# Performance work log

Hardware: AMD Instinct MI355X
Metric: run time of the kernel (lower is better)

The kernel has to match this reference:

```python
import jax, jax.numpy as jnp
import numpy as np

TAU = 1.0
NUM_CENTROIDS = 8
COMMITMENT_COST = 0.25


def setup_inputs() -> dict:
    key = jax.random.key(0)
    kx, kc = jax.random.split(key)
    B, T, D = 8, 2048, 512
    K = 4096  # codebook_size
    x = jax.random.normal(kx, (B, T, D), dtype=jnp.float32)
    # variance_scaling(1.0, fan_in, uniform): limit = sqrt(3/D)
    limit = np.sqrt(3.0 / D).astype(np.float32)
    codebook = jax.random.uniform(kc, (K, D), dtype=jnp.float32, minval=-limit, maxval=limit)
    return {"x": x, "codebook": codebook}


def _squared_euclidean_distance(a, b):
    # a: [N, D], b: [K, D] -> [N, K]
    a2 = jnp.sum(a * a, axis=-1, keepdims=True)          # [N, 1]
    b2 = jnp.sum(b * b, axis=-1)                          # [K]
    ab = a @ b.T                                          # [N, K]
    return a2 - 2.0 * ab + b2


def reference(x, codebook):
    B, T, D = x.shape
    K = codebook.shape[0]
    flat = x.reshape(-1, D)
    distances = _squared_euclidean_distance(flat, codebook).reshape(B, T, K)
    weights = jax.nn.softmax(-distances / TAU, axis=-1)
    top_weights, top_indices = jax.lax.top_k(weights, NUM_CENTROIDS)  # [B,T,k]
    top_weights = top_weights / jnp.sum(top_weights, axis=-1, keepdims=True)
    # decode_ids: weighted sum of gathered codebook rows (== one-hot einsum)
    gathered = jnp.take(codebook, top_indices, axis=0)                # [B,T,k,D]
    quantized = jnp.einsum('btk,btkd->btd', top_weights, gathered)
    # train=True losses (entropy_loss_ratio == 0 -> skipped)
    e_latent_loss = jnp.mean((jax.lax.stop_gradient(quantized) - x) ** 2) * COMMITMENT_COST
    q_latent_loss = jnp.mean((quantized - jax.lax.stop_gradient(x)) ** 2)
    loss = e_latent_loss.astype(jnp.float32) + q_latent_loss.astype(jnp.float32)
    # straight-through estimator
    quantized = x + jax.lax.stop_gradient(quantized - x)
    return quantized, loss
```

## Files before the change

### kernel.cpp

```cpp
#include <hip/hip_runtime.h>
#include <hip/hip_bf16.h>
#include <stdint.h>

#define D_DIM 512
#define K_CB  4096
#define N_TOK 16384
#define TOPK  8

#define TOKB  64
#define NPASS 4

typedef __attribute__((ext_vector_type(8)))  short          bf16x8;
typedef __attribute__((ext_vector_type(8)))  unsigned short us8;
typedef __attribute__((ext_vector_type(16))) float          f32x16;
typedef __attribute__((ext_vector_type(4)))  float          f32x4;

__device__ __forceinline__ unsigned short f2bf(float f) {
    union { float f; unsigned u; } v; v.f = f;
    unsigned r = (v.u + 0x7fffu + ((v.u >> 16) & 1u)) >> 16;
    return (unsigned short)r;
}

__device__ __forceinline__ void inskey(unsigned int k, unsigned int (&ts)[8]) {
    #pragma unroll
    for (int q = 0; q < 8; ++q) {
        unsigned int hi = ts[q] > k ? ts[q] : k;
        unsigned int lo = ts[q] > k ? k : ts[q];
        ts[q] = hi; k = lo;
    }
}

__global__ __launch_bounds__(256) void conv_cb_kernel(
    const float* __restrict__ cb, unsigned short* __restrict__ cbf,
    float* __restrict__ cnorm, float* __restrict__ loss,
    unsigned int* __restrict__ ticket) {
    __shared__ unsigned short ls[32 * 512];
    const int t = threadIdx.x, g32 = blockIdx.x;
    if (g32 == 0 && t == 0) { *loss = 0.f; *ticket = 0u; }
    const int row32 = t >> 3;
    float sq = 0.f;
    #pragma unroll
    for (int i = 0; i < 8; ++i) {
        const int gg = (t & 7) + 8 * i;
        const float* src = cb + ((size_t)(g32 * 32 + row32)) * D_DIM + gg * 8;
        float4 a = ((const float4*)src)[0], b = ((const float4*)src)[1];
        ushort4 o0, o1;
        o0.x = f2bf(a.x); o0.y = f2bf(a.y); o0.z = f2bf(a.z); o0.w = f2bf(a.w);
        o1.x = f2bf(b.x); o1.y = f2bf(b.y); o1.z = f2bf(b.z); o1.w = f2bf(b.w);
        const int li = (gg >> 1) * 512 + ((gg & 1) * 32 + row32) * 8;
        *(ushort4*)&ls[li]     = o0;
        *(ushort4*)&ls[li + 4] = o1;
        sq += a.x*a.x + a.y*a.y + a.z*a.z + a.w*a.w
            + b.x*b.x + b.y*b.y + b.z*b.z + b.w*b.w;
    }
    sq += __shfl_down(sq, 4, 8);
    sq += __shfl_down(sq, 2, 8);
    sq += __shfl_down(sq, 1, 8);
    if ((t & 7) == 0) cnorm[g32 * 32 + row32] = sq;
    __syncthreads();
    #pragma unroll
    for (int j = 0; j < 8; ++j) {
        const int s = j * 256 + t;
        *(ushort4*)(cbf + (size_t)g32 * 16384 + s * 8)     = *(const ushort4*)&ls[s * 8];
        *(ushort4*)(cbf + (size_t)g32 * 16384 + s * 8 + 4) = *(const ushort4*)&ls[s * 8 + 4];
    }
}

__global__ __launch_bounds__(1024) void vq_fused(
    const float* __restrict__ x, const float* __restrict__ cb,
    const unsigned short* __restrict__ cbf, const float* __restrict__ cnorm,
    float* __restrict__ out, float* __restrict__ loss_acc,
    unsigned int* __restrict__ ticket)
{
    __shared__ union {
        unsigned short xs[TOKB * D_DIM];
        unsigned int keys[256 * 64];
    } u;
    __shared__ float ncn[K_CB];
    __shared__ unsigned int pk[64 * 32];
    __shared__ int   tki[TOKB * TOPK];
    __shared__ float tks[TOKB * TOPK];
    __shared__ float tkw[TOKB * TOPK];
    __shared__ float redbuf[16];

    const int t    = threadIdx.x;
    const int lane = t & 63;
    const int w    = t >> 6;
    const int m32  = lane & 31;
    const int half = lane >> 5;
    const int tok0 = blockIdx.x * TOKB;

    #pragma unroll
    for (int i = 0; i < 2; ++i) {
        const int gg0 = i * 32 + w * 2;
        const float* src = x + (size_t)(tok0 + lane) * D_DIM + gg0 * 8;
        f32x4 v0 = ((const f32x4*)src)[0], v1 = ((const f32x4*)src)[1];
        f32x4 v2 = ((const f32x4*)src)[2], v3 = ((const f32x4*)src)[3];
        us8 o0, o1;
        o0[0] = f2bf(2.f*v0.x); o0[1] = f2bf(2.f*v0.y); o0[2] = f2bf(2.f*v0.z); o0[3] = f2bf(2.f*v0.w);
        o0[4] = f2bf(2.f*v1.x); o0[5] = f2bf(2.f*v1.y); o0[6] = f2bf(2.f*v1.z); o0[7] = f2bf(2.f*v1.w);
        o1[0] = f2bf(2.f*v2.x); o1[1] = f2bf(2.f*v2.y); o1[2] = f2bf(2.f*v2.z); o1[3] = f2bf(2.f*v2.w);
        o1[4] = f2bf(2.f*v3.x); o1[5] = f2bf(2.f*v3.y); o1[6] = f2bf(2.f*v3.z); o1[7] = f2bf(2.f*v3.w);
        const int di = (lane >> 5) * 16384 + (gg0 >> 1) * 512 + (lane & 31) * 8;
        *(us8*)&u.xs[di]       = o0;
        *(us8*)&u.xs[di + 256] = o1;
    }
    {
        float4 v = ((const float4*)cnorm)[t];
        float4 nv = {64.f - v.x, 64.f - v.y, 64.f - v.z, 64.f - v.w};
        *(float4*)&ncn[t * 4] = nv;
    }
    __syncthreads();

    unsigned int ts0[8], ts1[8];
    #pragma unroll
    for (int i = 0; i < 8; ++i) { ts0[i] = 0u; ts1[i] = 0u; }

    const char* cf = (const char*)cbf;
    for (int p = 0; p < NPASS; ++p) {
        const int ga = p * 32 + w * 2;
        f32x16 a00, a01, a10, a11;
        #pragma unroll
        for (int g = 0; g < 4; ++g) {
            float4 n0 = *(const float4*)&ncn[ga * 32 + g * 8 + 4 * half];
            float4 n1 = *(const float4*)&ncn[ga * 32 + 32 + g * 8 + 4 * half];
            a00[g*4+0]=n0.x; a00[g*4+1]=n0.y; a00[g*4+2]=n0.z; a00[g*4+3]=n0.w;
            a01[g*4+0]=n0.x; a01[g*4+1]=n0.y; a01[g*4+2]=n0.z; a01[g*4+3]=n0.w;
            a10[g*4+0]=n1.x; a10[g*4+1]=n1.y; a10[g*4+2]=n1.z; a10[g*4+3]=n1.w;
            a11[g*4+0]=n1.x; a11[g*4+1]=n1.y; a11[g*4+2]=n1.z; a11[g*4+3]=n1.w;
        }
        const char* ab = cf + (size_t)ga * 32768 + (size_t)lane * 16;
        #pragma unroll 8
        for (int ks = 0; ks < 32; ++ks) {
            bf16x8 A0 = *(const bf16x8*)(ab + (size_t)ks * 1024);
            bf16x8 A1 = *(const bf16x8*)(ab + 32768 + (size_t)ks * 1024);
            bf16x8 B0 = *(const bf16x8*)&u.xs[ks * 512 + lane * 8];
            bf16x8 B1 = *(const bf16x8*)&u.xs[16384 + ks * 512 + lane * 8];
            a00 = __builtin_amdgcn_mfma_f32_32x32x16_bf16(A0, B0, a00, 0, 0, 0);
            a01 = __builtin_amdgcn_mfma_f32_32x32x16_bf16(A0, B1, a01, 0, 0, 0);
            a10 = __builtin_amdgcn_mfma_f32_32x32x16_bf16(A1, B0, a10, 0, 0, 0);
            a11 = __builtin_amdgcn_mfma_f32_32x32x16_bf16(A1, B1, a11, 0, 0, 0);
        }
        const unsigned int K0 = 4095u - (unsigned int)(ga * 32) - 4u * (unsigned int)half;
        #pragma unroll
        for (int r = 0; r < 16; ++r) {
            const unsigned int cr = (unsigned int)((r & 3) + 8 * (r >> 2));
            inskey((__float_as_uint(a00[r]) & 0xFFFFF000u) | (K0 - cr),       ts0);
            inskey((__float_as_uint(a01[r]) & 0xFFFFF000u) | (K0 - cr),       ts1);
            inskey((__float_as_uint(a10[r]) & 0xFFFFF000u) | (K0 - 32u - cr), ts0);
            inskey((__float_as_uint(a11[r]) & 0xFFFFF000u) | (K0 - 32u - cr), ts1);
        }
    }

    __syncthreads();
    {
        const int kk = (w * 2 + half) * 8;
        #pragma unroll
        for (int e = 0; e < 8; ++e) {
            u.keys[(kk + e) * 64 + m32]      = ts0[e];
            u.keys[(kk + e) * 64 + 32 + m32] = ts1[e];
        }
    }
    __syncthreads();
    if (t < 256) {
        const int token = t >> 2, sub = t & 3;
        unsigned int bs[8];
        #pragma unroll
        for (int i = 0; i < 8; ++i) bs[i] = 0u;
        #pragma unroll 4
        for (int k = 0; k < 64; ++k) inskey(u.keys[(sub * 64 + k) * 64 + token], bs);
        #pragma unroll
        for (int e = 0; e < 8; ++e) pk[token * 32 + sub * 8 + e] = bs[e];
    }
    __syncthreads();
    if (t < TOKB) {
        unsigned int bs[8];
        #pragma unroll
        for (int i = 0; i < 8; ++i) bs[i] = 0u;
        #pragma unroll 4
        for (int k = 0; k < 32; ++k) inskey(pk[t * 32 + k], bs);
        #pragma unroll
        for (int r = 0; r < TOPK; ++r) tki[t * TOPK + r] = 4095 - (int)(bs[r] & 0xFFFu);
    }
    __syncthreads();
    {
        const int token = t >> 4, e = (t >> 1) & 7, dh = t & 1;
        const int idx = tki[token * TOPK + e];
        const float4* xr = (const float4*)(x + (size_t)(tok0 + token) * D_DIM) + dh * 64;
        const float4* cr = (const float4*)(cb + (size_t)idx * D_DIM) + dh * 64;
        float dot = 0.f;
        #pragma unroll 4
        for (int i = 0; i < 64; ++i) {
            float4 xv = xr[i], cv = cr[i];
            dot += xv.x*cv.x + xv.y*cv.y + xv.z*cv.z + xv.w*cv.w;
        }
        dot += __shfl_xor(dot, 1, 64);
        if (dh == 0) tks[token * TOPK + e] = 2.f * dot - cnorm[idx];
    }
    __syncthreads();
    if (t < TOKB) {
        float m = -1e38f;
        #pragma unroll
        for (int e = 0; e < TOPK; ++e) m = fmaxf(m, tks[t*TOPK+e]);
        float sum = 0.f, wv[TOPK];
        #pragma unroll
        for (int e = 0; e < TOPK; ++e) { wv[e] = __expf(tks[t*TOPK+e] - m); sum += wv[e]; }
        const float inv = 1.f / sum;
        #pragma unroll
        for (int e = 0; e < TOPK; ++e) tkw[t*TOPK+e] = wv[e] * inv;
    }
    __syncthreads();
    float lsum = 0.f;
    #pragma unroll 1
    for (int it = 0; it < (TOKB * (D_DIM / 4)) / 1024; ++it) {
        const int p = it * 1024 + t;
        const int token = p >> 7, d4 = p & 127;
        float4 q = {0.f, 0.f, 0.f, 0.f};
        #pragma unroll
        for (int e = 0; e < TOPK; ++e) {
            const float wv = tkw[token * TOPK + e];
            const int  idx = tki[token * TOPK + e];
            const float4 cv = ((const float4*)cb)[(size_t)idx * (D_DIM / 4) + d4];
            q.x += wv * cv.x; q.y += wv * cv.y; q.z += wv * cv.z; q.w += wv * cv.w;
        }
        const size_t go = (size_t)(tok0 + token) * (D_DIM / 4) + d4;
        f32x4 xv = __builtin_nontemporal_load((const f32x4*)x + go);
        const float ex = q.x - xv.x, ey = q.y - xv.y, ez = q.z - xv.z, ew = q.w - xv.w;
        lsum += ex*ex + ey*ey + ez*ez + ew*ew;
        f32x4 qv = {q.x, q.y, q.z, q.w};
        __builtin_nontemporal_store(qv, (f32x4*)out + go);
    }
    #pragma unroll
    for (int off = 32; off > 0; off >>= 1) lsum += __shfl_down(lsum, off, 64);
    if (lane == 0) redbuf[w] = lsum;
    __syncthreads();
    if (t == 0) {
        float s = 0.f;
        #pragma unroll
        for (int i = 0; i < 16; ++i) s += redbuf[i];
        atomicAdd(loss_acc, s);
        __threadfence();
        unsigned int prev = atomicAdd(ticket, 1u);
        if (prev == (unsigned int)(gridDim.x - 1)) {
            __threadfence();
            float total = atomicAdd(loss_acc, 0.f);
            out[(size_t)N_TOK * D_DIM] = 1.25f * total / (float)((size_t)N_TOK * D_DIM);
        }
    }
}

extern "C" void kernel_launch(void* const* d_in, const int* in_sizes, int n_in,
                              void* d_out, int out_size, void* d_ws, size_t ws_size,
                              hipStream_t stream) {
    const float* x  = (const float*)d_in[0];
    const float* cb = (const float*)d_in[1];
    float* out = (float*)d_out;

    char* ws = (char*)d_ws;
    unsigned short* cbf    = (unsigned short*)ws;
    float*          cnorm  = (float*)(ws + 4194304);
    float*          loss   = (float*)(ws + 4210688);
    unsigned int*   ticket = (unsigned int*)(ws + 4210752);

    conv_cb_kernel<<<128, 256, 0, stream>>>(cb, cbf, cnorm, loss, ticket);
    vq_fused<<<N_TOK / TOKB, 1024, 0, stream>>>(x, cb, cbf, cnorm, out, loss, ticket);
}
```

Before: 255.4 us.

## Switch distance GEMM to scaled FP8 MFMA with 16-candidate fp32 rerank

Result: slower. 285.7 us (+11.9%).

```diff
diff --git a/kernel.cpp b/kernel.cpp
--- a/kernel.cpp
+++ b/kernel.cpp
@@ -1,5 +1,4 @@
 #include <hip/hip_runtime.h>
-#include <hip/hip_bf16.h>
 #include <stdint.h>
 
 #define D_DIM 512
@@ -9,21 +8,17 @@
 
 #define TOKB  64
 #define NPASS 4
-
-typedef __attribute__((ext_vector_type(8)))  short          bf16x8;
-typedef __attribute__((ext_vector_type(8)))  unsigned short us8;
-typedef __attribute__((ext_vector_type(16))) float          f32x16;
-typedef __attribute__((ext_vector_type(4)))  float          f32x4;
-
-__device__ __forceinline__ unsigned short f2bf(float f) {
-    union { float f; unsigned u; } v; v.f = f;
-    unsigned r = (v.u + 0x7fffu + ((v.u >> 16) & 1u)) >> 16;
-    return (unsigned short)r;
-}
-
-__device__ __forceinline__ void inskey(unsigned int k, unsigned int (&ts)[8]) {
+#define NSEL  16
+
+typedef __attribute__((ext_vector_type(4)))  int    i32x4;
+typedef __attribute__((ext_vector_type(8)))  int    i32x8;
+typedef __attribute__((ext_vector_type(16))) float  f32x16;
+typedef __attribute__((ext_vector_type(4)))  float  f32x4;
+
+template<int N>
+__device__ __forceinline__ void inskey(unsigned int k, unsigned int (&ts)[N]) {
     #pragma unroll
-    for (int q = 0; q < 8; ++q) {
+    for (int q = 0; q < N; ++q) {
         unsigned int hi = ts[q] > k ? ts[q] : k;
         unsigned int lo = ts[q] > k ? k : ts[q];
         ts[q] = hi; k = lo;
@@ -31,56 +26,54 @@
 }
 
 __global__ __launch_bounds__(256) void conv_cb_kernel(
-    const float* __restrict__ cb, unsigned short* __restrict__ cbf,
+    const float* __restrict__ cb, unsigned char* __restrict__ cbf8,
     float* __restrict__ cnorm, float* __restrict__ loss,
     unsigned int* __restrict__ ticket) {
-    __shared__ unsigned short ls[32 * 512];
-    const int t = threadIdx.x, g32 = blockIdx.x;
-    if (g32 == 0 && t == 0) { *loss = 0.f; *ticket = 0u; }
-    const int row32 = t >> 3;
+    const int t = threadIdx.x, g = blockIdx.x;
+    if (g == 0 && t == 0) { *loss = 0.f; *ticket = 0u; }
+    const int r = t >> 3, s = t & 7;
+    const float* src = cb + ((size_t)(g * 32 + r)) * D_DIM + s * 64;
     float sq = 0.f;
+    unsigned int d[16];
     #pragma unroll
-    for (int i = 0; i < 8; ++i) {
-        const int gg = (t & 7) + 8 * i;
-        const float* src = cb + ((size_t)(g32 * 32 + row32)) * D_DIM + gg * 8;
-        float4 a = ((const float4*)src)[0], b = ((const float4*)src)[1];
-        ushort4 o0, o1;
-        o0.x = f2bf(a.x); o0.y = f2bf(a.y); o0.z = f2bf(a.z); o0.w = f2bf(a.w);
-        o1.x = f2bf(b.x); o1.y = f2bf(b.y); o1.z = f2bf(b.z); o1.w = f2bf(b.w);
-        const int li = (gg >> 1) * 512 + ((gg & 1) * 32 + row32) * 8;
-        *(ushort4*)&ls[li]     = o0;
-        *(ushort4*)&ls[li + 4] = o1;
-        sq += a.x*a.x + a.y*a.y + a.z*a.z + a.w*a.w
-            + b.x*b.x + b.y*b.y + b.z*b.z + b.w*b.w;
+    for (int i = 0; i < 16; ++i) {
+        float4 v = ((const float4*)src)[i];
+        sq += v.x*v.x + v.y*v.y + v.z*v.z + v.w*v.w;
+        int dd = __builtin_amdgcn_cvt_pk_fp8_f32(64.f * v.x, 64.f * v.y, 0, false);
+        dd     = __builtin_amdgcn_cvt_pk_fp8_f32(64.f * v.z, 64.f * v.w, dd, true);
+        d[i] = (unsigned int)dd;
     }
     sq += __shfl_down(sq, 4, 8);
     sq += __shfl_down(sq, 2, 8);
     sq += __shfl_down(sq, 1, 8);
-    if ((t & 7) == 0) cnorm[g32 * 32 + row32] = sq;
-    __syncthreads();
-    #pragma unroll
-    for (int j = 0; j < 8; ++j) {
-        const int s = j * 256 + t;
-        *(ushort4*)(cbf + (size_t)g32 * 16384 + s * 8)     = *(const ushort4*)&ls[s * 8];
-        *(ushort4*)(cbf + (size_t)g32 * 16384 + s * 8 + 4) = *(const ushort4*)&ls[s * 8 + 4];
-    }
+    if (s == 0) cnorm[g * 32 + r] = sq;
+    unsigned char* dst = cbf8 + (size_t)g * 16384 + (size_t)s * 2048;
+    i32x4 w0 = {(int)d[0],  (int)d[1],  (int)d[2],  (int)d[3]};
+    i32x4 w1 = {(int)d[4],  (int)d[5],  (int)d[6],  (int)d[7]};
+    i32x4 w2 = {(int)d[8],  (int)d[9],  (int)d[10], (int)d[11]};
+    i32x4 w3 = {(int)d[12], (int)d[13], (int)d[14], (int)d[15]};
+    *(i32x4*)(dst +        (size_t)r * 16)        = w0;
+    *(i32x4*)(dst + 1024 + (size_t)r * 16)        = w1;
+    *(i32x4*)(dst +        (size_t)(32 + r) * 16) = w2;
+    *(i32x4*)(dst + 1024 + (size_t)(32 + r) * 16) = w3;
 }
 
 __global__ __launch_bounds__(1024) void vq_fused(
     const float* __restrict__ x, const float* __restrict__ cb,
-    const unsigned short* __restrict__ cbf, const float* __restrict__ cnorm,
+    const unsigned char* __restrict__ cbf8, const float* __restrict__ cnorm,
     float* __restrict__ out, float* __restrict__ loss_acc,
     unsigned int* __restrict__ ticket)
 {
     __shared__ union {
-        unsigned short xs[TOKB * D_DIM];
-        unsigned int keys[256 * 64];
+        unsigned char xs8[TOKB * D_DIM];
+        unsigned int  keys[256 * 64];
     } u;
     __shared__ float ncn[K_CB];
-    __shared__ unsigned int pk[64 * 32];
-    __shared__ int   tki[TOKB * TOPK];
-    __shared__ float tks[TOKB * TOPK];
+    __shared__ unsigned int pk[64 * 64];
+    __shared__ int   tki[TOKB * NSEL];
+    __shared__ float tks[TOKB * NSEL];
     __shared__ float tkw[TOKB * TOPK];
+    __shared__ int   tkif[TOKB * TOPK];
     __shared__ float redbuf[16];
 
     const int t    = threadIdx.x;
@@ -90,24 +83,29 @@
     const int half = lane >> 5;
     const int tok0 = blockIdx.x * TOKB;
 
-    #pragma unroll
-    for (int i = 0; i < 2; ++i) {
-        const int gg0 = i * 32 + w * 2;
-        const float* src = x + (size_t)(tok0 + lane) * D_DIM + gg0 * 8;
-        f32x4 v0 = ((const f32x4*)src)[0], v1 = ((const f32x4*)src)[1];
-        f32x4 v2 = ((const f32x4*)src)[2], v3 = ((const f32x4*)src)[3];
-        us8 o0, o1;
-        o0[0] = f2bf(2.f*v0.x); o0[1] = f2bf(2.f*v0.y); o0[2] = f2bf(2.f*v0.z); o0[3] = f2bf(2.f*v0.w);
-        o0[4] = f2bf(2.f*v1.x); o0[5] = f2bf(2.f*v1.y); o0[6] = f2bf(2.f*v1.z); o0[7] = f2bf(2.f*v1.w);
-        o1[0] = f2bf(2.f*v2.x); o1[1] = f2bf(2.f*v2.y); o1[2] = f2bf(2.f*v2.z); o1[3] = f2bf(2.f*v2.w);
-        o1[4] = f2bf(2.f*v3.x); o1[5] = f2bf(2.f*v3.y); o1[6] = f2bf(2.f*v3.z); o1[7] = f2bf(2.f*v3.w);
-        const int di = (lane >> 5) * 16384 + (gg0 >> 1) * 512 + (lane & 31) * 8;
-        *(us8*)&u.xs[di]       = o0;
-        *(us8*)&u.xs[di + 256] = o1;
+    {
+        const int token = t >> 4, c = t & 15;
+        const int s2 = c >> 1, lh = c & 1;
+        const f32x4* src = (const f32x4*)(x + (size_t)(tok0 + token) * D_DIM + c * 32);
+        unsigned int d[8];
+        #pragma unroll
+        for (int i = 0; i < 8; ++i) {
+            f32x4 v = src[i];
+            int dd = __builtin_amdgcn_cvt_pk_fp8_f32(16.f * v.x, 16.f * v.y, 0, false);
+            dd     = __builtin_amdgcn_cvt_pk_fp8_f32(16.f * v.z, 16.f * v.w, dd, true);
+            d[i] = (unsigned int)dd;
+        }
+        const int lf = lh * 32 + (token & 31);
+        unsigned char* base = u.xs8 + (token >> 5) * 16384 + s2 * 2048 + lf * 16;
+        i32x4 lo = {(int)d[0], (int)d[1], (int)d[2], (int)d[3]};
+        i32x4 hi = {(int)d[4], (int)d[5], (int)d[6], (int)d[7]};
+        *(i32x4*)(base)        = lo;
+        *(i32x4*)(base + 1024) = hi;
     }
     {
         float4 v = ((const float4*)cnorm)[t];
-        float4 nv = {64.f - v.x, 64.f - v.y, 64.f - v.z, 64.f - v.w};
+        float4 nv = {32768.f - 512.f * v.x, 32768.f - 512.f * v.y,
+                     32768.f - 512.f * v.z, 32768.f - 512.f * v.w};
         *(float4*)&ncn[t * 4] = nv;
     }
     __syncthreads();
@@ -116,8 +114,11 @@
     #pragma unroll
     for (int i = 0; i < 8; ++i) { ts0[i] = 0u; ts1[i] = 0u; }
 
-    const char* cf = (const char*)cbf;
-    for (int p = 0; p < NPASS; ++p) {
+    const char* ab0 = (const char*)cbf8 + (size_t)(w * 2) * 16384 + (size_t)lane * 16;
+    const unsigned char* pb = u.xs8 + lane * 16;
+
+    for (int pp = 0; pp < NPASS; ++pp) {
+        const int p  = (pp + w) & 3;
         const int ga = p * 32 + w * 2;
         f32x16 a00, a01, a10, a11;
         #pragma unroll
@@ -129,18 +130,32 @@
             a10[g*4+0]=n1.x; a10[g*4+1]=n1.y; a10[g*4+2]=n1.z; a10[g*4+3]=n1.w;
             a11[g*4+0]=n1.x; a11[g*4+1]=n1.y; a11[g*4+2]=n1.z; a11[g*4+3]=n1.w;
         }
-        const char* ab = cf + (size_t)ga * 32768 + (size_t)lane * 16;
-        #pragma unroll 8
-        for (int ks = 0; ks < 32; ++ks) {
-            bf16x8 A0 = *(const bf16x8*)(ab + (size_t)ks * 1024);
-            bf16x8 A1 = *(const bf16x8*)(ab + 32768 + (size_t)ks * 1024);
-            bf16x8 B0 = *(const bf16x8*)&u.xs[ks * 512 + lane * 8];
-            bf16x8 B1 = *(const bf16x8*)&u.xs[16384 + ks * 512 + lane * 8];
-            a00 = __builtin_amdgcn_mfma_f32_32x32x16_bf16(A0, B0, a00, 0, 0, 0);
-            a01 = __builtin_amdgcn_mfma_f32_32x32x16_bf16(A0, B1, a01, 0, 0, 0);
-            a10 = __builtin_amdgcn_mfma_f32_32x32x16_bf16(A1, B0, a10, 0, 0, 0);
-            a11 = __builtin_amdgcn_mfma_f32_32x32x16_bf16(A1, B1, a11, 0, 0, 0);
-        }
+        const char* ab = ab0 + (size_t)p * 524288;
+        __builtin_amdgcn_s_setprio(1);
+        #pragma unroll
+        for (int s = 0; s < 8; ++s) {
+            i32x4 al0 = *(const i32x4*)(ab + s * 2048);
+            i32x4 ah0 = *(const i32x4*)(ab + s * 2048 + 1024);
+            i32x4 al1 = *(const i32x4*)(ab + s * 2048 + 16384);
+            i32x4 ah1 = *(const i32x4*)(ab + s * 2048 + 17408);
+            i32x4 bl0 = *(const i32x4*)(pb + s * 2048);
+            i32x4 bh0 = *(const i32x4*)(pb + s * 2048 + 1024);
+            i32x4 bl1 = *(const i32x4*)(pb + s * 2048 + 16384);
+            i32x4 bh1 = *(const i32x4*)(pb + s * 2048 + 17408);
+            i32x8 A0 = __builtin_shufflevector(al0, ah0, 0,1,2,3,4,5,6,7);
+            i32x8 A1 = __builtin_shufflevector(al1, ah1, 0,1,2,3,4,5,6,7);
+            i32x8 B0 = __builtin_shufflevector(bl0, bh0, 0,1,2,3,4,5,6,7);
+            i32x8 B1 = __builtin_shufflevector(bl1, bh1, 0,1,2,3,4,5,6,7);
+            a00 = __builtin_amdgcn_mfma_scale_f32_32x32x64_f8f6f4(
+                      A0, B0, a00, 0, 0, 0, 0x7F7F7F7F, 0, 0x7F7F7F7F);
+            a01 = __builtin_amdgcn_mfma_scale_f32_32x32x64_f8f6f4(
+                      A0, B1, a01, 0, 0, 0, 0x7F7F7F7F, 0, 0x7F7F7F7F);
+            a10 = __builtin_amdgcn_mfma_scale_f32_32x32x64_f8f6f4(
+                      A1, B0, a10, 0, 0, 0, 0x7F7F7F7F, 0, 0x7F7F7F7F);
+            a11 = __builtin_amdgcn_mfma_scale_f32_32x32x64_f8f6f4(
+                      A1, B1, a11, 0, 0, 0, 0x7F7F7F7F, 0, 0x7F7F7F7F);
+        }
+        __builtin_amdgcn_s_setprio(0);
         const unsigned int K0 = 4095u - (unsigned int)(ga * 32) - 4u * (unsigned int)half;
         #pragma unroll
         for (int r = 0; r < 16; ++r) {
@@ -164,50 +179,87 @@
     __syncthreads();
     if (t < 256) {
         const int token = t >> 2, sub = t & 3;
-        unsigned int bs[8];
-        #pragma unroll
-        for (int i = 0; i < 8; ++i) bs[i] = 0u;
-        #pragma unroll 4
+        unsigned int bs[16];
+        #pragma unroll
+        for (int i = 0; i < 16; ++i) bs[i] = 0u;
+        #pragma unroll 2
         for (int k = 0; k < 64; ++k) inskey(u.keys[(sub * 64 + k) * 64 + token], bs);
         #pragma unroll
-        for (int e = 0; e < 8; ++e) pk[token * 32 + sub * 8 + e] = bs[e];
+        for (int e = 0; e < 16; ++e) pk[token * 64 + sub * 16 + e] = bs[e];
+    }
+    __syncthreads();
+    if (t < TOKB) {
+        unsigned int bs[NSEL];
+        #pragma unroll
+        for (int i = 0; i < NSEL; ++i) bs[i] = 0u;
+        #pragma unroll 2
+        for (int k = 0; k < 64; ++k) inskey(pk[t * 64 + k], bs);
+        #pragma unroll
+        for (int r = 0; r < NSEL; ++r) tki[t * NSEL + r] = 4095 - (int)(bs[r] & 0xFFFu);
+    }
+    __syncthreads();
+    {
+        const int token = t >> 4, sl = t & 15;
+        const f32x4* xr = (const f32x4*)(x + (size_t)(tok0 + token) * D_DIM);
+        f32x4 xv[8];
+        #pragma unroll
+        for (int i = 0; i < 8; ++i) xv[i] = xr[sl + 16 * i];
+        #pragma unroll
+        for (int hh = 0; hh < 2; ++hh) {
+            float pd[8];
+            #pragma unroll
+            for (int e = 0; e < 8; ++e) {
+                const int idx = tki[token * NSEL + hh * 8 + e];
+                const f32x4* cr = (const f32x4*)(cb + (size_t)idx * D_DIM);
+                float dot = 0.f;
+                #pragma unroll
+                for (int i = 0; i < 8; ++i) {
+                    f32x4 cv = cr[sl + 16 * i];
+                    dot += xv[i].x*cv.x + xv[i].y*cv.y + xv[i].z*cv.z + xv[i].w*cv.w;
+                }
+                pd[e] = dot;
+            }
+            #pragma unroll
+            for (int e = 0; e < 8; ++e) {
+                pd[e] += __shfl_down(pd[e], 8, 16);
+                pd[e] += __shfl_down(pd[e], 4, 16);
+                pd[e] += __shfl_down(pd[e], 2, 16);
+                pd[e] += __shfl_down(pd[e], 1, 16);
+            }
+            if (sl == 0) {
+                #pragma unroll
+                for (int e = 0; e < 8; ++e)
+                    tks[token * NSEL + hh * 8 + e] =
+                        2.f * pd[e] - cnorm[tki[token * NSEL + hh * 8 + e]];
+            }
+        }
     }
     __syncthreads();
     if (t < TOKB) {
         unsigned int bs[8];
         #pragma unroll
         for (int i = 0; i < 8; ++i) bs[i] = 0u;
-        #pragma unroll 4
-        for (int k = 0; k < 32; ++k) inskey(pk[t * 32 + k], bs);
-        #pragma unroll
-        for (int r = 0; r < TOPK; ++r) tki[t * TOPK + r] = 4095 - (int)(bs[r] & 0xFFFu);
-    }
-    __syncthreads();
-    {
-        const int token = t >> 4, e = (t >> 1) & 7, dh = t & 1;
-        const int idx = tki[token * TOPK + e];
-        const float4* xr = (const float4*)(x + (size_t)(tok0 + token) * D_DIM) + dh * 64;
-        const float4* cr = (const float4*)(cb + (size_t)idx * D_DIM) + dh * 64;
-        float dot = 0.f;
-        #pragma unroll 4
-        for (int i = 0; i < 64; ++i) {
-            float4 xv = xr[i], cv = cr[i];
-            dot += xv.x*cv.x + xv.y*cv.y + xv.z*cv.z + xv.w*cv.w;
-        }
-        dot += __shfl_xor(dot, 1, 64);
-        if (dh == 0) tks[token * TOPK + e] = 2.f * dot - cnorm[idx];
-    }
-    __syncthreads();
-    if (t < TOKB) {
-        float m = -1e38f;
-        #pragma unroll
-        for (int e = 0; e < TOPK; ++e) m = fmaxf(m, tks[t*TOPK+e]);
-        float sum = 0.f, wv[TOPK];
-        #pragma unroll
-        for (int e = 0; e < TOPK; ++e) { wv[e] = __expf(tks[t*TOPK+e] - m); sum += wv[e]; }
+        #pragma unroll
+        for (int e = 0; e < NSEL; ++e) {
+            unsigned int uu = __float_as_uint(tks[t * NSEL + e]);
+            uu ^= (unsigned int)((int)uu >> 31) | 0x80000000u;
+            inskey((uu & 0xFFFFFFF0u) | (unsigned int)e, bs);
+        }
+        const float m = tks[t * NSEL + (int)(bs[0] & 15u)];
+        float wv[TOPK], sum = 0.f;
+        int ids[TOPK];
+        #pragma unroll
+        for (int r = 0; r < TOPK; ++r) {
+            const int e = (int)(bs[r] & 15u);
+            wv[r] = __expf(tks[t * NSEL + e] - m); sum += wv[r];
+            ids[r] = tki[t * NSEL + e];
+        }
         const float inv = 1.f / sum;
         #pragma unroll
-        for (int e = 0; e < TOPK; ++e) tkw[t*TOPK+e] = wv[e] * inv;
+        for (int r = 0; r < TOPK; ++r) {
+            tkw[t * TOPK + r] = wv[r] * inv;
+            tkif[t * TOPK + r] = ids[r];
+        }
     }
     __syncthreads();
     float lsum = 0.f;
@@ -219,7 +271,7 @@
         #pragma unroll
         for (int e = 0; e < TOPK; ++e) {
             const float wv = tkw[token * TOPK + e];
-            const int  idx = tki[token * TOPK + e];
+            const int  idx = tkif[token * TOPK + e];
             const float4 cv = ((const float4*)cb)[(size_t)idx * (D_DIM / 4) + d4];
             q.x += wv * cv.x; q.y += wv * cv.y; q.z += wv * cv.z; q.w += wv * cv.w;
         }
@@ -257,11 +309,11 @@
     float* out = (float*)d_out;
 
     char* ws = (char*)d_ws;
-    unsigned short* cbf    = (unsigned short*)ws;
-    float*          cnorm  = (float*)(ws + 4194304);
-    float*          loss   = (float*)(ws + 4210688);
-    unsigned int*   ticket = (unsigned int*)(ws + 4210752);
-
-    conv_cb_kernel<<<128, 256, 0, stream>>>(cb, cbf, cnorm, loss, ticket);
-    vq_fused<<<N_TOK / TOKB, 1024, 0, stream>>>(x, cb, cbf, cnorm, out, loss, ticket);
+    unsigned char* cbf8   = (unsigned char*)ws;
+    float*         cnorm  = (float*)(ws + 2097152);
+    float*         loss   = (float*)(ws + 2113536);
+    unsigned int*  ticket = (unsigned int*)(ws + 2113600);
+
+    conv_cb_kernel<<<128, 256, 0, stream>>>(cb, cbf8, cnorm, loss, ticket);
+    vq_fused<<<N_TOK / TOKB, 1024, 0, stream>>>(x, cb, cbf8, cnorm, out, loss, ticket);
 }
```
